# Kernel optimization log

Hardware: AMD Instinct MI355X
Metric: run time of the kernel (lower is better)

The kernel has to match this reference:

```python
import jax, jax.numpy as jnp
import numpy as np

B, D, F, S, R = 2048, 1024, 1024, 64, 16


def _lora_dense(x, ids, kernel, bias, la, lb):
    # base: frozen dense path (stop_gradient mirrors the original module)
    base = x @ jax.lax.stop_gradient(kernel)
    if bias is not None:
        base = base + jax.lax.stop_gradient(bias)
    a = la[ids]            # (B, D, R) per-example adapter gather
    b = lb[ids]            # (B, R, F)
    low = jnp.einsum('bd,bdr->br', x, a)
    delta = jnp.einsum('br,brf->bf', low, b)
    return base + delta


def setup_inputs() -> dict:
    key = jax.random.key(0)
    ks = jax.random.split(key, 32)
    i = iter(range(32))
    d = {}
    d['carry'] = jax.random.normal(ks[next(i)], (B, F), jnp.float32)
    d['inputs'] = jax.random.normal(ks[next(i)], (B, D), jnp.float32)
    d['adapter_ids'] = jax.random.randint(ks[next(i)], (B,), 0, S)
    kscale = 1.0 / np.sqrt(D)
    for g in ['ir', 'iu', 'ic']:
        d[f'w_{g}'] = jax.random.normal(ks[next(i)], (D, F), jnp.float32) * kscale
        d[f'bias_{g}'] = jax.random.normal(ks[next(i)], (F,), jnp.float32) * 0.01
        d[f'la_{g}'] = jax.random.normal(ks[next(i)], (S, D, R), jnp.float32) * 0.02
        d[f'lb_{g}'] = jax.random.normal(ks[next(i)], (S, R, F), jnp.float32) * 0.01
    for g in ['rr', 'ru', 'rc']:
        d[f'w_{g}'] = jax.random.normal(ks[next(i)], (F, F), jnp.float32) * kscale
        d[f'la_{g}'] = jax.random.normal(ks[next(i)], (S, F, R), jnp.float32) * 0.02
        d[f'lb_{g}'] = jax.random.normal(ks[next(i)], (S, R, F), jnp.float32) * 0.01
    return d


def reference(carry, inputs, adapter_ids,
              w_ir, bias_ir, la_ir, lb_ir,
              w_iu, bias_iu, la_iu, lb_iu,
              w_ic, bias_ic, la_ic, lb_ic,
              w_rr, la_rr, lb_rr,
              w_ru, la_ru, lb_ru,
              w_rc, la_rc, lb_rc):
    ids = adapter_ids
    reset = jax.nn.sigmoid(
        _lora_dense(inputs, ids, w_ir, bias_ir, la_ir, lb_ir)
        + _lora_dense(carry, ids, w_rr, None, la_rr, lb_rr))
    update = jax.nn.sigmoid(
        _lora_dense(inputs, ids, w_iu, bias_iu, la_iu, lb_iu)
        + _lora_dense(carry, ids, w_ru, None, la_ru, lb_ru))
    candidate = jnp.tanh(
        _lora_dense(inputs, ids, w_ic, bias_ic, la_ic, lb_ic)
        + reset * _lora_dense(carry, ids, w_rc, None, la_rc, lb_rc))
    new_carry = (1.0 - update) * candidate + update * carry
    return new_carry
```

## Files before the change

### kernel.cpp

```cpp
#include <hip/hip_runtime.h>
#include <stdint.h>

#define B_  2048
#define D_  1024
#define F_  1024
#define S_  64
#define R_  16

typedef __attribute__((ext_vector_type(8))) short  s16x8;
typedef __attribute__((ext_vector_type(4))) unsigned short u16x4;
typedef __attribute__((ext_vector_type(8))) unsigned short u16x8;
typedef __attribute__((ext_vector_type(4))) float  f32x4;

__device__ __forceinline__ unsigned short f2b(float f){
  unsigned u = __float_as_uint(f);
  u = u + 0x7fffu + ((u >> 16) & 1u);
  return (unsigned short)(u >> 16);
}
__device__ __forceinline__ float b2f(unsigned short s){
  return __uint_as_float(((unsigned)s) << 16);
}

__device__ __forceinline__ void gload16(const void* g, void* l){
  __builtin_amdgcn_global_load_lds((const __attribute__((address_space(1))) unsigned int*)g,
                                   (__attribute__((address_space(3))) unsigned int*)l, 16, 0, 0);
}


__global__ __launch_bounds__(256) void prep_kernel(
    const float* __restrict__ x, const float* __restrict__ carry,
    unsigned short* __restrict__ XC,
    const float* __restrict__ w_ir, const float* __restrict__ w_rr,
    const float* __restrict__ w_iu, const float* __restrict__ w_ru,
    const float* __restrict__ w_ic, const float* __restrict__ w_rc,
    unsigned short* __restrict__ Wt_all,
    const int* __restrict__ ids, int* __restrict__ starts, int* __restrict__ order){
  int bx = blockIdx.x;
  int t = threadIdx.x;
  if (bx < 2048){
    int i = bx * 256 + t;
    int b = i >> 8;
    int j = (i & 255) * 4;
    float4 xv = *(const float4*)&x[(size_t)b*D_ + j];
    float4 cv = *(const float4*)&carry[(size_t)b*F_ + j];
    u16x4 xs, cs;
    xs[0]=f2b(xv.x); xs[1]=f2b(xv.y); xs[2]=f2b(xv.z); xs[3]=f2b(xv.w);
    cs[0]=f2b(cv.x); cs[1]=f2b(cv.y); cs[2]=f2b(cv.z); cs[3]=f2b(cv.w);
    *(u16x4*)&XC[(size_t)b*2048 + j]        = xs;
    *(u16x4*)&XC[(size_t)b*2048 + 1024 + j] = cs;
    return;
  }
  if (bx < 3584){
    int wb = bx - 2048;
    int g = wb >> 8, xb = wb & 255;
    const float* W;
    switch(g){ case 0: W=w_ir; break; case 1: W=w_rr; break; case 2: W=w_iu; break;
               case 3: W=w_ru; break; case 4: W=w_ic; break; default: W=w_rc; break; }
    unsigned short* O = Wt_all + (size_t)g * 1048576;
    __shared__ unsigned short T[64][72];
    int n0 = (xb & 15) * 64;
    int k0 = (xb >> 4) * 64;
    int c4 = (t & 15) * 4;
    int kk = t >> 4;
    #pragma unroll
    for (int i = 0; i < 4; i++){
      int k = kk + i*16;
      float4 v = *(const float4*)&W[(size_t)(k0+k)*F_ + n0 + c4];
      T[c4+0][k] = f2b(v.x); T[c4+1][k] = f2b(v.y); T[c4+2][k] = f2b(v.z); T[c4+3][k] = f2b(v.w);
    }
    __syncthreads();
    int n = t >> 2, ch = (t & 3) * 16;
    u16x8 a = *(const u16x8*)&T[n][ch];
    u16x8 b = *(const u16x8*)&T[n][ch+8];
    *(u16x8*)&O[(size_t)(n0+n)*1024 + k0 + ch]     = a;
    *(u16x8*)&O[(size_t)(n0+n)*1024 + k0 + ch + 8] = b;
    return;
  }
  __shared__ int cnt[S_]; __shared__ int off[S_+1]; __shared__ int cur[S_];
  if (t < S_) cnt[t] = 0;
  __syncthreads();
  for (int b = t; b < B_; b += 256) atomicAdd(&cnt[ids[b]], 1);
  __syncthreads();
  if (t == 0){ off[0] = 0; for (int s2 = 0; s2 < S_; s2++) off[s2+1] = off[s2] + cnt[s2]; }
  __syncthreads();
  if (t < S_) cur[t] = off[t];
  __syncthreads();
  for (int b = t; b < B_; b += 256){ int p = atomicAdd(&cur[ids[b]], 1); order[p] = b; }
  if (t < S_+1) starts[t] = off[t];
}

__global__ __launch_bounds__(256, 4) void gemm_low_kernel(
    const unsigned short* __restrict__ XC,
    const unsigned short* __restrict__ Wt_all,
    unsigned short* __restrict__ Yall,
    const float* __restrict__ la_ir, const float* __restrict__ la_iu,
    const float* __restrict__ la_ic, const float* __restrict__ la_rr,
    const float* __restrict__ la_ru, const float* __restrict__ la_rc,
    const int* __restrict__ starts, const int* __restrict__ order,
    unsigned short* __restrict__ lowb){
  __shared__ __align__(16) unsigned short smem[16512];
  int t = threadIdx.x;
  int bx = blockIdx.x;

  if (bx < 384){
    int s = bx & 63, g = bx >> 6;
    const float* la;
    switch(g){ case 0: la=la_ir; break; case 1: la=la_iu; break; case 2: la=la_ic; break;
               case 3: la=la_rr; break; case 4: la=la_ru; break; default: la=la_rc; break; }
    int kofs = (g < 3) ? 0 : 1024;
    la += (size_t)s * D_ * R_;
    unsigned short* LA = smem;
    for (int i4 = t; i4 < D_*R_/4; i4 += 256){
      float4 v = *(const float4*)&la[i4*4];
      int d = i4 >> 2, r0 = (i4 & 3) * 4;
      LA[(r0+0)*1032 + d] = f2b(v.x);
      LA[(r0+1)*1032 + d] = f2b(v.y);
      LA[(r0+2)*1032 + d] = f2b(v.z);
      LA[(r0+3)*1032 + d] = f2b(v.w);
    }
    __syncthreads();
    int start = starts[s], cnt = starts[s+1] - start;
    if (cnt == 0) return;
    int lane = t & 63, wave = t >> 6;
    int l15 = lane & 15, kq = (lane >> 4) * 8;
    int ntiles = (cnt + 15) >> 4;
    for (int mt = wave; mt < ntiles; mt += 4){
      int m0 = mt*16 + l15; if (m0 >= cnt) m0 = cnt - 1;
      int e0 = order[start + m0];
      const unsigned short* A0 = XC + (size_t)e0*2048 + kofs + kq;
      const unsigned short* Bp = &LA[l15*1032 + kq];
      f32x4 accA = {}, accB = {};
      #pragma unroll 4
      for (int kt = 0; kt < 512; kt += 32){
        s16x8 a0 = *(const s16x8*)(A0 + kt);
        s16x8 b0 = *(const s16x8*)(Bp + kt);
        s16x8 a1 = *(const s16x8*)(A0 + 512 + kt);
        s16x8 b1 = *(const s16x8*)(Bp + 512 + kt);
        accA = __builtin_amdgcn_mfma_f32_16x16x32_bf16(a0, b0, accA, 0, 0, 0);
        accB = __builtin_amdgcn_mfma_f32_16x16x32_bf16(a1, b1, accB, 0, 0, 0);
      }
      f32x4 acc = accA + accB;
      int rowb = (lane >> 4) * 4;
      #pragma unroll
      for (int i = 0; i < 4; i++){
        int m = mt*16 + rowb + i;
        if (m < cnt){
          int e = order[start + m];
          lowb[((size_t)g*B_ + e)*R_ + l15] = f2b(acc[i]);
        }
      }
    }
    return;
  }

  int bid = bx - 384;
  int u = bid >> 7;
  int tile = bid & 127;
  int kofs = (u & 1) << 10;
  const unsigned short* Wt = Wt_all + (size_t)u * 1048576;
  unsigned short* Y = Yall + (size_t)u * ((size_t)B_ * F_);

  unsigned short (*As)[4096] = (unsigned short(*)[4096])smem;
  unsigned short (*Bs)[4096] = (unsigned short(*)[4096])(smem + 8192);

  int lane = t & 63, wave = t >> 6;
  int mt = tile >> 3, nt = tile & 7;
  int row0 = mt * 128, col0 = nt * 128;
  int wrow = (wave >> 1) * 64, wcol = (wave & 1) * 64;

  int arow = t >> 2;
  int achk = ((t & 3) ^ ((t >> 3) & 3)) * 8;

  const unsigned short* Ab  = XC + (size_t)(row0 + arow) * 2048 + kofs + achk;
  const unsigned short* Ab2 = Ab + (size_t)64 * 2048;
  const unsigned short* Bb  = Wt + (size_t)(col0 + arow) * 1024 + achk;
  const unsigned short* Bb2 = Bb + (size_t)64 * 1024;

  int l15 = lane & 15;
  int kof = (((lane >> 4) ^ ((l15 >> 1) & 3)) * 8);
  f32x4 acc[4][4] = {};

  gload16(Ab,  &As[0][t*8]);  gload16(Ab2, &As[0][2048 + t*8]);
  gload16(Bb,  &Bs[0][t*8]);  gload16(Bb2, &Bs[0][2048 + t*8]);
  __syncthreads();

  int cur = 0;
  for (int kt = 32; kt < 1024; kt += 32){
    int nxt = cur ^ 1;
    gload16(Ab  + kt, &As[nxt][t*8]);  gload16(Ab2 + kt, &As[nxt][2048 + t*8]);
    gload16(Bb  + kt, &Bs[nxt][t*8]);  gload16(Bb2 + kt, &Bs[nxt][2048 + t*8]);
    s16x8 af[4], bfr[4];
    #pragma unroll
    for (int m = 0; m < 4; m++)
      af[m] = *(const s16x8*)&As[cur][(wrow + m*16 + l15)*32 + kof];
    #pragma unroll
    for (int n = 0; n < 4; n++)
      bfr[n] = *(const s16x8*)&Bs[cur][(wcol + n*16 + l15)*32 + kof];
    __builtin_amdgcn_s_setprio(1);
    #pragma unroll
    for (int m = 0; m < 4; m++){
      #pragma unroll
      for (int n = 0; n < 4; n++){
        acc[m][n] = __builtin_amdgcn_mfma_f32_16x16x32_bf16(af[m], bfr[n], acc[m][n], 0, 0, 0);
      }
    }
    __builtin_amdgcn_s_setprio(0);
    __syncthreads();
    cur = nxt;
  }
  {
    s16x8 af[4], bfr[4];
    #pragma unroll
    for (int m = 0; m < 4; m++)
      af[m] = *(const s16x8*)&As[cur][(wrow + m*16 + l15)*32 + kof];
    #pragma unroll
    for (int n = 0; n < 4; n++)
      bfr[n] = *(const s16x8*)&Bs[cur][(wcol + n*16 + l15)*32 + kof];
    #pragma unroll
    for (int m = 0; m < 4; m++){
      #pragma unroll
      for (int n = 0; n < 4; n++){
        acc[m][n] = __builtin_amdgcn_mfma_f32_16x16x32_bf16(af[m], bfr[n], acc[m][n], 0, 0, 0);
      }
    }
  }

  int orow = row0 + wrow + (lane >> 4) * 4;
  int ocol = col0 + wcol + l15;
  #pragma unroll
  for (int m = 0; m < 4; m++){
    #pragma unroll
    for (int n = 0; n < 4; n++){
      #pragma unroll
      for (int i = 0; i < 4; i++){
        Y[(size_t)(orow + m*16 + i) * F_ + ocol + n*16] = f2b(acc[m][n][i]);
      }
    }
  }
}

__global__ __launch_bounds__(256) void delta_final_kernel(
    const float* __restrict__ carry,
    const float* __restrict__ bias_ir, const float* __restrict__ bias_iu,
    const float* __restrict__ bias_ic,
    const float* __restrict__ lb_ir, const float* __restrict__ lb_rr,
    const float* __restrict__ lb_iu, const float* __restrict__ lb_ru,
    const float* __restrict__ lb_ic, const float* __restrict__ lb_rc,
    const int* __restrict__ starts, const int* __restrict__ order,
    const unsigned short* __restrict__ lowb, const unsigned short* __restrict__ Yall,
    float* __restrict__ out){
  int s = blockIdx.x;
  int c0 = blockIdx.y * 128;
  __shared__ unsigned short Bsm[3 * 128 * 40];
  int t = threadIdx.x;
  const float* lbp[6] = {lb_ir, lb_rr, lb_iu, lb_ru, lb_ic, lb_rc};
  #pragma unroll
  for (int j = 0; j < 6; j++){
    const float* lb = lbp[j] + (size_t)s * R_ * F_;
    unsigned short* Bj = &Bsm[(j >> 1)*5120 + (j & 1)*16];
    #pragma unroll
    for (int it = 0; it < 2; it++){
      int idx = t + it*256;
      int r = idx >> 5, c4 = (idx & 31) * 4;
      float4 v = *(const float4*)&lb[(size_t)r*F_ + c0 + c4];
      Bj[(c4+0)*40 + r] = f2b(v.x);
      Bj[(c4+1)*40 + r] = f2b(v.y);
      Bj[(c4+2)*40 + r] = f2b(v.z);
      Bj[(c4+3)*40 + r] = f2b(v.w);
    }
  }
  __syncthreads();
  int start = starts[s], cnt = starts[s+1] - start;
  if (cnt == 0) return;
  int lane = t & 63, wave = t >> 6;
  int l15 = lane & 15, kq = (lane >> 4) * 8;
  int ntiles = (cnt + 15) >> 4;
  const unsigned short* Y0 = Yall + 0*(size_t)B_*F_;
  const unsigned short* Y1 = Yall + 1*(size_t)B_*F_;
  const unsigned short* Y2 = Yall + 2*(size_t)B_*F_;
  const unsigned short* Y3 = Yall + 3*(size_t)B_*F_;
  const unsigned short* Y4 = Yall + 4*(size_t)B_*F_;
  const unsigned short* Y5 = Yall + 5*(size_t)B_*F_;
  int k8 = kq & 15; bool hi = (kq >= 16);
  for (int pt = wave; pt < ntiles*2; pt += 4){
    int mt = pt >> 1, cf0 = (pt & 1) * 4;
    int m = mt*16 + l15; if (m >= cnt) m = cnt - 1;
    int e = order[start + m];
    s16x8 a_r, a_u, a_c1 = {}, a_c2 = {};
    a_r = *(const s16x8*)&lowb[((size_t)(hi ? 3 : 0)*B_ + e)*R_ + k8];
    a_u = *(const s16x8*)&lowb[((size_t)(hi ? 4 : 1)*B_ + e)*R_ + k8];
    if (!hi) a_c1 = *(const s16x8*)&lowb[((size_t)2*B_ + e)*R_ + k8];
    else     a_c2 = *(const s16x8*)&lowb[((size_t)5*B_ + e)*R_ + k8];
    int rowb = (lane >> 4) * 4;
    int erow[4]; bool wok[4];
    #pragma unroll
    for (int i = 0; i < 4; i++){
      int mm = mt*16 + rowb + i;
      wok[i] = (mm < cnt);
      erow[i] = order[start + (wok[i] ? mm : cnt - 1)];
    }
    #pragma unroll
    for (int cf = cf0; cf < cf0 + 4; cf++){
      int col = cf*16 + l15;
      s16x8 b_r = *(const s16x8*)&Bsm[0*5120 + col*40 + kq];
      s16x8 b_u = *(const s16x8*)&Bsm[1*5120 + col*40 + kq];
      s16x8 b_c = *(const s16x8*)&Bsm[2*5120 + col*40 + kq];
      f32x4 zero = {};
      f32x4 dr  = __builtin_amdgcn_mfma_f32_16x16x32_bf16(a_r,  b_r, zero, 0, 0, 0);
      f32x4 du  = __builtin_amdgcn_mfma_f32_16x16x32_bf16(a_u,  b_u, zero, 0, 0, 0);
      f32x4 dic = __builtin_amdgcn_mfma_f32_16x16x32_bf16(a_c1, b_c, zero, 0, 0, 0);
      f32x4 drc = __builtin_amdgcn_mfma_f32_16x16x32_bf16(a_c2, b_c, zero, 0, 0, 0);
      int oc = c0 + col;
      float br = bias_ir[oc], bu = bias_iu[oc], bc = bias_ic[oc];
      #pragma unroll
      for (int i = 0; i < 4; i++){
        if (wok[i]){
          size_t idx = (size_t)erow[i]*F_ + oc;
          float zr  = b2f(Y0[idx]) + b2f(Y1[idx]) + br + dr[i];
          float zu  = b2f(Y2[idx]) + b2f(Y3[idx]) + bu + du[i];
          float zic = b2f(Y4[idx]) + bc + dic[i];
          float zrc = b2f(Y5[idx]) + drc[i];
          float cv  = carry[idx];
          float rr = 1.f/(1.f+__expf(-zr));
          float uu = 1.f/(1.f+__expf(-zu));
          float a = zic + rr*zrc;
          float ee = __expf(-2.f*fabsf(a));
          float cand = copysignf((1.f-ee)/(1.f+ee), a);
          out[idx] = (1.f-uu)*cand + uu*cv;
        }
      }
    }
  }
}

extern "C" void kernel_launch(void* const* d_in, const int* in_sizes, int n_in,
                              void* d_out, int out_size, void* d_ws, size_t ws_size,
                              hipStream_t stream){
  const float* carry   = (const float*)d_in[0];
  const float* x       = (const float*)d_in[1];
  const int*   ids     = (const int*)d_in[2];
  const float* w_ir    = (const float*)d_in[3];
  const float* bias_ir = (const float*)d_in[4];
  const float* la_ir   = (const float*)d_in[5];
  const float* lb_ir   = (const float*)d_in[6];
  const float* w_iu    = (const float*)d_in[7];
  const float* bias_iu = (const float*)d_in[8];
  const float* la_iu   = (const float*)d_in[9];
  const float* lb_iu   = (const float*)d_in[10];
  const float* w_ic    = (const float*)d_in[11];
  const float* bias_ic = (const float*)d_in[12];
  const float* la_ic   = (const float*)d_in[13];
  const float* lb_ic   = (const float*)d_in[14];
  const float* w_rr    = (const float*)d_in[15];
  const float* la_rr   = (const float*)d_in[16];
  const float* lb_rr   = (const float*)d_in[17];
  const float* w_ru    = (const float*)d_in[18];
  const float* la_ru   = (const float*)d_in[19];
  const float* lb_ru   = (const float*)d_in[20];
  const float* w_rc    = (const float*)d_in[21];
  const float* la_rc   = (const float*)d_in[22];
  const float* lb_rc   = (const float*)d_in[23];

  char* ws = (char*)d_ws;
  unsigned short* XC     = (unsigned short*)(ws + 0);
  unsigned short* Wt_all = (unsigned short*)(ws + 8388608);
  unsigned short* Yall   = (unsigned short*)(ws + 20971520);
  unsigned short* lowb   = (unsigned short*)(ws + 46137344);
  int* starts = (int*)(ws + 46530560);
  int* order  = (int*)(ws + 46531584);

  prep_kernel<<<dim3(3585), dim3(256), 0, stream>>>(x, carry, XC,
                                                    w_ir, w_rr, w_iu, w_ru, w_ic, w_rc,
                                                    Wt_all, ids, starts, order);
  gemm_low_kernel<<<dim3(1152), dim3(256), 0, stream>>>(XC, Wt_all, Yall,
                                                        la_ir, la_iu, la_ic,
                                                        la_rr, la_ru, la_rc,
                                                        starts, order, lowb);
  delta_final_kernel<<<dim3(64, 8), dim3(256), 0, stream>>>(carry, bias_ir, bias_iu, bias_ic,
                                                            lb_ir, lb_rr, lb_iu, lb_ru,
                                                            lb_ic, lb_rc,
                                                            starts, order, lowb, Yall,
                                                            (float*)d_out);
}
```

Before: 89.85 us.

## Fuse input and recurrent GEMMs for reset/update gates via concatenated K

The reset and update gates now each run one GEMM with K=2048 over the concatenated [x, carry] activations against stacked [W_i; W_r] weights, instead of two K=1024 GEMMs whose outputs were added later. This cuts the stored bf16 intermediate outputs from six to four and removes two extra Y reads in the final kernel. The LoRA low-rank blocks are moved after the GEMM blocks in the grid. The trade-off is a less uniform grid (tiles with K=2048 take twice as long), which may leave an uneven tail at the end.

Measured after the change: 81.24 us. 9.6% less time.

```diff
diff --git a/kernel.cpp b/kernel.cpp
--- a/kernel.cpp
+++ b/kernel.cpp
@@ -25,6 +25,11 @@
   __builtin_amdgcn_global_load_lds((const __attribute__((address_space(1))) unsigned int*)g,
                                    (__attribute__((address_space(3))) unsigned int*)l, 16, 0, 0);
 }
+
+#define W0OFF 0
+#define W1OFF 2097152
+#define W2OFF 4194304
+#define W3OFF 5242880
 
 
 __global__ __launch_bounds__(256) void prep_kernel(
@@ -53,10 +58,15 @@
   if (bx < 3584){
     int wb = bx - 2048;
     int g = wb >> 8, xb = wb & 255;
-    const float* W;
-    switch(g){ case 0: W=w_ir; break; case 1: W=w_rr; break; case 2: W=w_iu; break;
-               case 3: W=w_ru; break; case 4: W=w_ic; break; default: W=w_rc; break; }
-    unsigned short* O = Wt_all + (size_t)g * 1048576;
+    const float* W; unsigned short* O; int st, ko;
+    switch(g){
+      case 0:  W=w_ir; O=Wt_all+W0OFF; st=2048; ko=0;    break;
+      case 1:  W=w_rr; O=Wt_all+W0OFF; st=2048; ko=1024; break;
+      case 2:  W=w_iu; O=Wt_all+W1OFF; st=2048; ko=0;    break;
+      case 3:  W=w_ru; O=Wt_all+W1OFF; st=2048; ko=1024; break;
+      case 4:  W=w_ic; O=Wt_all+W2OFF; st=1024; ko=0;    break;
+      default: W=w_rc; O=Wt_all+W3OFF; st=1024; ko=0;    break;
+    }
     __shared__ unsigned short T[64][72];
     int n0 = (xb & 15) * 64;
     int k0 = (xb >> 4) * 64;
@@ -72,8 +82,8 @@
     int n = t >> 2, ch = (t & 3) * 16;
     u16x8 a = *(const u16x8*)&T[n][ch];
     u16x8 b = *(const u16x8*)&T[n][ch+8];
-    *(u16x8*)&O[(size_t)(n0+n)*1024 + k0 + ch]     = a;
-    *(u16x8*)&O[(size_t)(n0+n)*1024 + k0 + ch + 8] = b;
+    *(u16x8*)&O[(size_t)(n0+n)*st + ko + k0 + ch]     = a;
+    *(u16x8*)&O[(size_t)(n0+n)*st + ko + k0 + ch + 8] = b;
     return;
   }
   __shared__ int cnt[S_]; __shared__ int off[S_+1]; __shared__ int cur[S_];
@@ -102,8 +112,9 @@
   int t = threadIdx.x;
   int bx = blockIdx.x;
 
-  if (bx < 384){
-    int s = bx & 63, g = bx >> 6;
+  if (bx >= 512){
+    int lb = bx - 512;
+    int s = lb & 63, g = lb >> 6;
     const float* la;
     switch(g){ case 0: la=la_ir; break; case 1: la=la_iu; break; case 2: la=la_ic; break;
                case 3: la=la_rr; break; case 4: la=la_ru; break; default: la=la_rc; break; }
@@ -153,11 +164,12 @@
     return;
   }
 
-  int bid = bx - 384;
-  int u = bid >> 7;
-  int tile = bid & 127;
-  int kofs = (u & 1) << 10;
-  const unsigned short* Wt = Wt_all + (size_t)u * 1048576;
+  int u = bx >> 7;
+  int tile = bx & 127;
+  int K = (u < 2) ? 2048 : 1024;
+  int kofs = (u == 3) ? 1024 : 0;
+  const size_t uoffs[4] = {W0OFF, W1OFF, W2OFF, W3OFF};
+  const unsigned short* Wt = Wt_all + uoffs[u];
   unsigned short* Y = Yall + (size_t)u * ((size_t)B_ * F_);
 
   unsigned short (*As)[4096] = (unsigned short(*)[4096])smem;
@@ -173,8 +185,8 @@
 
   const unsigned short* Ab  = XC + (size_t)(row0 + arow) * 2048 + kofs + achk;
   const unsigned short* Ab2 = Ab + (size_t)64 * 2048;
-  const unsigned short* Bb  = Wt + (size_t)(col0 + arow) * 1024 + achk;
-  const unsigned short* Bb2 = Bb + (size_t)64 * 1024;
+  const unsigned short* Bb  = Wt + (size_t)(col0 + arow) * K + achk;
+  const unsigned short* Bb2 = Bb + (size_t)64 * K;
 
   int l15 = lane & 15;
   int kof = (((lane >> 4) ^ ((l15 >> 1) & 3)) * 8);
@@ -185,7 +197,7 @@
   __syncthreads();
 
   int cur = 0;
-  for (int kt = 32; kt < 1024; kt += 32){
+  for (int kt = 32; kt < K; kt += 32){
     int nxt = cur ^ 1;
     gload16(Ab  + kt, &As[nxt][t*8]);  gload16(Ab2 + kt, &As[nxt][2048 + t*8]);
     gload16(Bb  + kt, &Bs[nxt][t*8]);  gload16(Bb2 + kt, &Bs[nxt][2048 + t*8]);
@@ -279,8 +291,6 @@
   const unsigned short* Y1 = Yall + 1*(size_t)B_*F_;
   const unsigned short* Y2 = Yall + 2*(size_t)B_*F_;
   const unsigned short* Y3 = Yall + 3*(size_t)B_*F_;
-  const unsigned short* Y4 = Yall + 4*(size_t)B_*F_;
-  const unsigned short* Y5 = Yall + 5*(size_t)B_*F_;
   int k8 = kq & 15; bool hi = (kq >= 16);
   for (int pt = wave; pt < ntiles*2; pt += 4){
     int mt = pt >> 1, cf0 = (pt & 1) * 4;
@@ -316,10 +326,10 @@
       for (int i = 0; i < 4; i++){
         if (wok[i]){
           size_t idx = (size_t)erow[i]*F_ + oc;
-          float zr  = b2f(Y0[idx]) + b2f(Y1[idx]) + br + dr[i];
-          float zu  = b2f(Y2[idx]) + b2f(Y3[idx]) + bu + du[i];
-          float zic = b2f(Y4[idx]) + bc + dic[i];
-          float zrc = b2f(Y5[idx]) + drc[i];
+          float zr  = b2f(Y0[idx]) + br + dr[i];
+          float zu  = b2f(Y1[idx]) + bu + du[i];
+          float zic = b2f(Y2[idx]) + bc + dic[i];
+          float zrc = b2f(Y3[idx]) + drc[i];
           float cv  = carry[idx];
           float rr = 1.f/(1.f+__expf(-zr));
           float uu = 1.f/(1.f+__expf(-zu));
@@ -365,17 +375,17 @@
   unsigned short* XC     = (unsigned short*)(ws + 0);
   unsigned short* Wt_all = (unsigned short*)(ws + 8388608);
   unsigned short* Yall   = (unsigned short*)(ws + 20971520);
-  unsigned short* lowb   = (unsigned short*)(ws + 46137344);
-  int* starts = (int*)(ws + 46530560);
-  int* order  = (int*)(ws + 46531584);
+  unsigned short* lowb   = (unsigned short*)(ws + 37748736);
+  int* starts = (int*)(ws + 38141952);
+  int* order  = (int*)(ws + 38142976);
 
   prep_kernel<<<dim3(3585), dim3(256), 0, stream>>>(x, carry, XC,
                                                     w_ir, w_rr, w_iu, w_ru, w_ic, w_rc,
                                                     Wt_all, ids, starts, order);
-  gemm_low_kernel<<<dim3(1152), dim3(256), 0, stream>>>(XC, Wt_all, Yall,
-                                                        la_ir, la_iu, la_ic,
-                                                        la_rr, la_ru, la_rc,
-                                                        starts, order, lowb);
+  gemm_low_kernel<<<dim3(896), dim3(256), 0, stream>>>(XC, Wt_all, Yall,
+                                                       la_ir, la_iu, la_ic,
+                                                       la_rr, la_ru, la_rc,
+                                                       starts, order, lowb);
   delta_final_kernel<<<dim3(64, 8), dim3(256), 0, stream>>>(carry, bias_ir, bias_iu, bias_ic,
                                                             lb_ir, lb_rr, lb_iu, lb_ru,
                                                             lb_ic, lb_rc,
```
